# Optimization experiments

Hardware: AMD Instinct MI355X
Metric: run time of the kernel (lower is better)

## Reference

```python
import jax, jax.numpy as jnp
import numpy as np

N_NODES = 100000
N_EDGES = 1600000
IN_CH = 128
HID = 128
EPS = 1e-5


def setup_inputs() -> dict:
    key = jax.random.key(0)
    ks = jax.random.split(key, 16)
    x = jax.random.normal(ks[0], (N_NODES, IN_CH), dtype=jnp.float32)
    edge_index = jax.random.randint(ks[1], (2, N_EDGES), 0, N_NODES, dtype=jnp.int64)
    dims = [(IN_CH, HID), (HID, HID), (HID, HID // 2)]
    params = {}
    for i, (di, do) in enumerate(dims):
        params[f'w{i}'] = jax.random.normal(ks[2 + i], (di, do), dtype=jnp.float32) * (1.0 / np.sqrt(di))
        params[f'b{i}'] = jnp.zeros((do,), dtype=jnp.float32)
        params[f'g{i}'] = jnp.ones((do,), dtype=jnp.float32)
        params[f'be{i}'] = jnp.zeros((do,), dtype=jnp.float32)
    params['wc1'] = jax.random.normal(ks[8], (HID // 2, 32), dtype=jnp.float32) * (1.0 / np.sqrt(HID // 2))
    params['bc1'] = jnp.zeros((32,), dtype=jnp.float32)
    params['wc2'] = jax.random.normal(ks[9], (32, 1), dtype=jnp.float32) * (1.0 / np.sqrt(32))
    params['bc2'] = jnp.zeros((1,), dtype=jnp.float32)
    return {'x': x, 'edge_index': edge_index, **params}


def _gcn_forward(x, edge_index, w0, b0, g0, be0, w1, b1, g1, be1, w2, b2, g2, be2, wc1, bc1, wc2, bc2):
    n = x.shape[0]
    # add self-loops (GCNConv default)
    loops = jnp.arange(n, dtype=edge_index.dtype)
    src = jnp.concatenate([edge_index[0], loops])  # [E+N]
    dst = jnp.concatenate([edge_index[1], loops])
    # symmetric normalization: deg over targets (incl. self loops)
    deg = jax.ops.segment_sum(jnp.ones_like(dst, dtype=x.dtype), dst, num_segments=n)
    dis = jax.lax.rsqrt(jnp.maximum(deg, 1e-12))  # deg>=1 due to self loops
    norm = (dis[src] * dis[dst])[:, None]  # [E+N, 1]

    def layer(h, w, b, g, be):
        h = h @ w                                   # [N, d_out]
        h = jax.ops.segment_sum(h[src] * norm, dst, num_segments=n) + b
        mu = jnp.mean(h, axis=0)
        var = jnp.mean(jnp.square(h - mu), axis=0)  # biased var (torch BN)
        h = (h - mu) * jax.lax.rsqrt(var + EPS) * g + be
        return jax.nn.relu(h)                       # dropout: identity (eval)

    h = layer(x, w0, b0, g0, be0)
    h = layer(h, w1, b1, g1, be1)
    h = layer(h, w2, b2, g2, be2)
    h = jax.nn.relu(h @ wc1 + bc1)
    return (h @ wc2 + bc2)[:, 0]  # [N]


def reference(x, edge_index, w0, b0, g0, be0, w1, b1, g1, be1, w2, b2, g2, be2, wc1, bc1, wc2, bc2):
    return _gcn_forward(x, edge_index, w0, b0, g0, be0, w1, b1, g1, be1, w2, b2, g2, be2, wc1, bc1, wc2, bc2)
```

## Files before the change

### kernel.cpp

```cpp
#include <hip/hip_runtime.h>


typedef __attribute__((ext_vector_type(8))) short short8;
typedef __attribute__((ext_vector_type(4))) float f32x4;

#define BIN_SHIFT 7
#define BIN_NODES 128
#define CAPB 4096
#define CAP 64

__device__ __forceinline__ float b2f(unsigned short u) {
    return __uint_as_float(((unsigned)u) << 16);
}
__device__ __forceinline__ unsigned short f2bf(float f) {
    unsigned u = __float_as_uint(f);
    return (unsigned short)((u + 0x7fff + ((u >> 16) & 1)) >> 16);
}

__global__ __launch_bounds__(256) void part1_kernel(const int* __restrict__ eidx,
                                                    int E, int nbins, int chunk,
                                                    int* __restrict__ bin_fill,
                                                    int* __restrict__ binned) {
    __shared__ int cntS[1024];
    __shared__ int baseS[1024];
    int tid = threadIdx.x;
    for (int b = tid; b < nbins; b += 256) cntS[b] = 0;
    __syncthreads();
    int e0 = blockIdx.x * chunk;
    int e1 = min(e0 + chunk, E);
    for (int e = e0 + tid; e < e1; e += 256)
        atomicAdd(&cntS[eidx[E + e] >> BIN_SHIFT], 1);
    __syncthreads();
    for (int b = tid; b < nbins; b += 256) {
        baseS[b] = atomicAdd(&bin_fill[b], cntS[b]);
        cntS[b] = 0;
    }
    __syncthreads();
    for (int e = e0 + tid; e < e1; e += 256) {
        int d = eidx[E + e];
        int s = eidx[e];
        int b = d >> BIN_SHIFT;
        int p = baseS[b] + atomicAdd(&cntS[b], 1);
        if (p < CAPB) binned[b * CAPB + p] = (s << BIN_SHIFT) | (d & (BIN_NODES - 1));
    }
}

__global__ __launch_bounds__(256) void part2_kernel(const int* __restrict__ bin_fill,
                                                    const int* __restrict__ binned,
                                                    int N, int* __restrict__ fill,
                                                    float* __restrict__ dis,
                                                    int* __restrict__ stage) {
    __shared__ int lfill[BIN_NODES];
    int b = blockIdx.x, tid = threadIdx.x;
    if (tid < BIN_NODES) lfill[tid] = 0;
    __syncthreads();
    int cnt = min(bin_fill[b], CAPB);
    const int* seg = binned + b * CAPB;
    for (int i = tid; i < cnt; i += 256) {
        int v = seg[i];
        int dl = v & (BIN_NODES - 1);
        int p = atomicAdd(&lfill[dl], 1);
        int node = (b << BIN_SHIFT) + dl;
        if (p < CAP) stage[(node << 6) + p] = v >> BIN_SHIFT;
    }
    __syncthreads();
    if (tid < BIN_NODES) {
        int node = (b << BIN_SHIFT) + tid;
        if (node < N) {
            int c = lfill[tid];
            fill[node] = c;
            dis[node] = rsqrtf((float)c + 1.0f);
        }
    }
}

__global__ void wfrag_kernel(const float* __restrict__ w,
                             unsigned short* __restrict__ wf, int total, int C) {
    int tid = blockIdx.x * 256 + threadIdx.x;
    if (tid >= total) return;
    int j = tid & 7;
    int lane = (tid >> 3) & 63;
    int q = (tid >> 9) & 3;
    int n_tile = tid >> 11;
    int k = q * 32 + (lane >> 4) * 8 + j;
    int n = n_tile * 16 + (lane & 15);
    wf[tid] = f2bf(w[k * C + n]);
}

__device__ __forceinline__ void load8(const float* p, float4& lo, float4& hi) {
    lo = *(const float4*)p;
    hi = *(const float4*)(p + 4);
}
__device__ __forceinline__ void load8(const unsigned short* p, float4& lo, float4& hi) {
    int4 q = *(const int4*)p;
    lo = make_float4(__uint_as_float((unsigned)q.x << 16),
                     __uint_as_float((unsigned)q.x & 0xffff0000u),
                     __uint_as_float((unsigned)q.y << 16),
                     __uint_as_float((unsigned)q.y & 0xffff0000u));
    hi = make_float4(__uint_as_float((unsigned)q.z << 16),
                     __uint_as_float((unsigned)q.z & 0xffff0000u),
                     __uint_as_float((unsigned)q.w << 16),
                     __uint_as_float((unsigned)q.w & 0xffff0000u));
}

template <int C, typename InT>
__global__ __launch_bounds__(256, 5) void mfma_gemm_kernel(
    const InT* __restrict__ xin, const unsigned short* __restrict__ wf,
    const float* __restrict__ scale, const float* __restrict__ shift,
    const float* __restrict__ dis, unsigned short* __restrict__ out, int N) {
    constexpr int NT = C / 16;
    constexpr int WFRAGS = NT * 4 * 64;
    __shared__ short8 ws[WFRAGS];
    int tid = threadIdx.x;
    for (int i = tid; i < WFRAGS; i += 256) ws[i] = ((const short8*)wf)[i];

    int lane = tid & 63;
    int wave = tid >> 6;
    int m0 = blockIdx.x * 64 + wave * 16;
    int r15 = lane & 15, r4 = lane >> 4;
    f32x4 acc[NT];
#pragma unroll
    for (int t = 0; t < NT; t++) acc[t] = (f32x4){0.f, 0.f, 0.f, 0.f};
    int row0 = m0 + r15;
    int row0c = min(row0, N - 1);
    __syncthreads();

#pragma unroll
    for (int q = 0; q < 4; q++) {
        int kb = q * 32 + r4 * 8;
        float4 a0l, a0h;
        load8(xin + (size_t)row0c * 128 + kb, a0l, a0h);
        if (scale) {
            float4 scl = *(const float4*)&scale[kb];
            float4 sch = *(const float4*)&scale[kb + 4];
            float4 shl = *(const float4*)&shift[kb];
            float4 shh = *(const float4*)&shift[kb + 4];
            a0l.x = fmaxf(a0l.x * scl.x + shl.x, 0.f);
            a0l.y = fmaxf(a0l.y * scl.y + shl.y, 0.f);
            a0l.z = fmaxf(a0l.z * scl.z + shl.z, 0.f);
            a0l.w = fmaxf(a0l.w * scl.w + shl.w, 0.f);
            a0h.x = fmaxf(a0h.x * sch.x + shh.x, 0.f);
            a0h.y = fmaxf(a0h.y * sch.y + shh.y, 0.f);
            a0h.z = fmaxf(a0h.z * sch.z + shh.z, 0.f);
            a0h.w = fmaxf(a0h.w * sch.w + shh.w, 0.f);
        }
        short8 a0;
        a0[0] = (short)f2bf(a0l.x); a0[1] = (short)f2bf(a0l.y);
        a0[2] = (short)f2bf(a0l.z); a0[3] = (short)f2bf(a0l.w);
        a0[4] = (short)f2bf(a0h.x); a0[5] = (short)f2bf(a0h.y);
        a0[6] = (short)f2bf(a0h.z); a0[7] = (short)f2bf(a0h.w);
#pragma unroll
        for (int nt = 0; nt < NT; nt++) {
            short8 b = ws[(nt * 4 + q) * 64 + lane];
            acc[nt] = __builtin_amdgcn_mfma_f32_16x16x32_bf16(a0, b, acc[nt], 0, 0, 0);
        }
    }
    float d0r[4];
#pragma unroll
    for (int r = 0; r < 4; r++) {
        int rowa = m0 + r4 * 4 + r;
        d0r[r] = (rowa < N) ? dis[rowa] : 0.f;
    }
#pragma unroll
    for (int nt = 0; nt < NT; nt++) {
        int col = nt * 16 + r15;
#pragma unroll
        for (int r = 0; r < 4; r++) {
            int rowa = m0 + r4 * 4 + r;
            if (rowa < N) out[(size_t)rowa * C + col] = f2bf(acc[nt][r] * d0r[r]);
        }
    }
}

__global__ __launch_bounds__(256) void agg128_kernel(
    const unsigned short* __restrict__ h, const int* __restrict__ fill,
    const int* __restrict__ stage, const float* __restrict__ dis,
    unsigned short* __restrict__ out, int N) {
    int lane = threadIdx.x & 63;
    int node = blockIdx.x * 4 + (threadIdx.x >> 6);
    if (node >= N) return;
    float dn = dis[node];
    ushort2 sv = ((const ushort2*)(h + (size_t)node * 128))[lane];
    float2 acc = make_float2(b2f(sv.x), b2f(sv.y));
    int ne = min(fill[node], CAP);
    int pk = (lane < ne) ? stage[(node << 6) + lane] : 0;
    int j = 0;
    for (; j + 16 <= ne; j += 16) {
        ushort2 a[16];
#pragma unroll
        for (int t = 0; t < 16; t++) {
            int s = __builtin_amdgcn_readlane(pk, j + t);
            a[t] = ((const ushort2*)(h + (size_t)s * 128))[lane];
        }
#pragma unroll
        for (int t = 0; t < 16; t++) { acc.x += b2f(a[t].x); acc.y += b2f(a[t].y); }
    }
    for (; j + 8 <= ne; j += 8) {
        ushort2 a[8];
#pragma unroll
        for (int t = 0; t < 8; t++) {
            int s = __builtin_amdgcn_readlane(pk, j + t);
            a[t] = ((const ushort2*)(h + (size_t)s * 128))[lane];
        }
#pragma unroll
        for (int t = 0; t < 8; t++) { acc.x += b2f(a[t].x); acc.y += b2f(a[t].y); }
    }
    for (; j + 4 <= ne; j += 4) {
        ushort2 a[4];
#pragma unroll
        for (int t = 0; t < 4; t++) {
            int s = __builtin_amdgcn_readlane(pk, j + t);
            a[t] = ((const ushort2*)(h + (size_t)s * 128))[lane];
        }
#pragma unroll
        for (int t = 0; t < 4; t++) { acc.x += b2f(a[t].x); acc.y += b2f(a[t].y); }
    }
    for (; j < ne; j++) {
        int s = __builtin_amdgcn_readlane(pk, j);
        ushort2 a = ((const ushort2*)(h + (size_t)s * 128))[lane];
        acc.x += b2f(a.x);
        acc.y += b2f(a.y);
    }
    ((ushort2*)(out + (size_t)node * 128))[lane] =
        make_ushort2(f2bf(acc.x * dn), f2bf(acc.y * dn));
}

__global__ __launch_bounds__(256) void agg64_kernel(
    const unsigned short* __restrict__ h, const int* __restrict__ fill,
    const int* __restrict__ stage, const float* __restrict__ dis,
    unsigned short* __restrict__ out, int N) {
    int lane = threadIdx.x & 63;
    int node = blockIdx.x * 4 + (threadIdx.x >> 6);
    if (node >= N) return;
    int half = lane >> 5, ch = lane & 31;
    float dn = dis[node];
    float2 acc = make_float2(0.f, 0.f);
    if (half == 0) {
        ushort2 sv = ((const ushort2*)(h + (size_t)node * 64))[ch];
        acc.x = b2f(sv.x);
        acc.y = b2f(sv.y);
    }
    int ne = min(fill[node], CAP);
    int pk = (lane < ne) ? stage[(node << 6) + lane] : 0;
    int j = 0;
    for (; j + 16 <= ne; j += 16) {
        ushort2 a[8];
#pragma unroll
        for (int t = 0; t < 8; t++) {
            int s = __shfl(pk, j + 2 * t + half);
            a[t] = ((const ushort2*)(h + (size_t)s * 64))[ch];
        }
#pragma unroll
        for (int t = 0; t < 8; t++) { acc.x += b2f(a[t].x); acc.y += b2f(a[t].y); }
    }
    for (; j + 8 <= ne; j += 8) {
        ushort2 a[4];
#pragma unroll
        for (int t = 0; t < 4; t++) {
            int s = __shfl(pk, j + 2 * t + half);
            a[t] = ((const ushort2*)(h + (size_t)s * 64))[ch];
        }
#pragma unroll
        for (int t = 0; t < 4; t++) { acc.x += b2f(a[t].x); acc.y += b2f(a[t].y); }
    }
    for (; j < ne; j += 2) {
        int jj = j + half;
        int s = __shfl(pk, jj);
        bool v = jj < ne;
        ushort2 a = ((const ushort2*)(h + (size_t)s * 64))[ch];
        acc.x += v ? b2f(a.x) : 0.f;
        acc.y += v ? b2f(a.y) : 0.f;
    }
    acc.x += __shfl_down(acc.x, 32);
    acc.y += __shfl_down(acc.y, 32);
    if (half == 0)
        ((ushort2*)(out + (size_t)node * 64))[ch] =
            make_ushort2(f2bf(acc.x * dn), f2bf(acc.y * dn));
}

template <int C>
__global__ __launch_bounds__(256) void stats_kernel(const unsigned short* __restrict__ h,
                                                    int N, float* __restrict__ sums) {
    constexpr int R = 256 / C;
    int c = threadIdx.x % C;
    int rg = threadIdx.x / C;
    float s = 0.f, s2 = 0.f;
    for (int n = blockIdx.x * R + rg; n < N; n += gridDim.x * R) {
        float v = b2f(h[(size_t)n * C + c]);
        s += v;
        s2 += v * v;
    }
    __shared__ float red[256], red2[256];
    red[threadIdx.x] = s;
    red2[threadIdx.x] = s2;
    __syncthreads();
    if (rg == 0) {
#pragma unroll
        for (int r = 1; r < R; r++) {
            s += red[r * C + c];
            s2 += red2[r * C + c];
        }
        atomicAdd(&sums[c], s);
        atomicAdd(&sums[C + c], s2);
    }
}

template <int C>
__global__ void finalize_kernel(const float* __restrict__ sums,
                                const float* __restrict__ g,
                                const float* __restrict__ be, int N,
                                float* __restrict__ scale, float* __restrict__ shift) {
    int c = threadIdx.x;
    float inv_n = 1.0f / (float)N;
    float mean = sums[c] * inv_n;
    float var = sums[C + c] * inv_n - mean * mean;
    var = var > 0.f ? var : 0.f;
    float sc = g[c] * rsqrtf(var + 1e-5f);
    scale[c] = sc;
    shift[c] = be[c] - mean * sc;
}

__global__ __launch_bounds__(256) void head_kernel(
    const unsigned short* __restrict__ h, const float* __restrict__ scale,
    const float* __restrict__ shift, const float* __restrict__ wc1,
    const float* __restrict__ bc1, const float* __restrict__ wc2,
    const float* __restrict__ bc2, float* __restrict__ out, int N) {
    __shared__ float w1s[64 * 32];
    __shared__ float b1s[32], w2s[32], s2s[64], sh2[64];
    __shared__ float b2s;
    int tid = threadIdx.x;
    for (int i = tid; i < 64 * 32; i += 256) w1s[i] = wc1[i];
    if (tid < 32) { b1s[tid] = bc1[tid]; w2s[tid] = wc2[tid]; }
    if (tid < 64) { s2s[tid] = scale[tid]; sh2[tid] = shift[tid]; }
    if (tid == 0) b2s = bc2[0];
    __syncthreads();
    int n = blockIdx.x * 256 + tid;
    if (n >= N) return;
    float v[64];
#pragma unroll
    for (int k = 0; k < 64; k++) {
        float x = b2f(h[(size_t)n * 64 + k]) * s2s[k] + sh2[k];
        v[k] = x > 0.f ? x : 0.f;
    }
    float o = b2s;
#pragma unroll 2
    for (int j = 0; j < 32; j++) {
        float t = b1s[j];
#pragma unroll
        for (int k = 0; k < 64; k++) t += v[k] * w1s[k * 32 + j];
        t = t > 0.f ? t : 0.f;
        o += t * w2s[j];
    }
    out[n] = o;
}

extern "C" void kernel_launch(void* const* d_in, const int* in_sizes, int n_in,
                              void* d_out, int out_size, void* d_ws, size_t ws_size,
                              hipStream_t stream) {
    const float* x = (const float*)d_in[0];
    const int* eidx = (const int*)d_in[1];
    const float* w0 = (const float*)d_in[2];
    const float* g0 = (const float*)d_in[4];
    const float* be0 = (const float*)d_in[5];
    const float* w1 = (const float*)d_in[6];
    const float* g1 = (const float*)d_in[8];
    const float* be1 = (const float*)d_in[9];
    const float* w2 = (const float*)d_in[10];
    const float* g2 = (const float*)d_in[12];
    const float* be2 = (const float*)d_in[13];
    const float* wc1 = (const float*)d_in[14];
    const float* bc1 = (const float*)d_in[15];
    const float* wc2 = (const float*)d_in[16];
    const float* bc2 = (const float*)d_in[17];

    const int N = in_sizes[0] / 128;
    const int E = in_sizes[1] / 2;
    const int nbins = (N + BIN_NODES - 1) >> BIN_SHIFT;

    char* p = (char*)d_ws;
    auto alloc = [&](size_t bytes) {
        void* r = (void*)p;
        p += (bytes + 255) & ~(size_t)255;
        return r;
    };
    float* sums = (float*)alloc(3 * 256 * 4);
    int* bin_fill = (int*)alloc((size_t)nbins * 4);
    size_t zero_bytes = (size_t)(p - (char*)d_ws);
    int* fill = (int*)alloc((size_t)N * 4);
    int* binned = (int*)alloc((size_t)nbins * CAPB * 4);
    int* stage = (int*)alloc((size_t)N * CAP * 4);
    float* dis = (float*)alloc((size_t)N * 4);
    float* ss = (float*)alloc(3 * 256 * 4);
    unsigned short* hA = (unsigned short*)alloc((size_t)N * 128 * 2);
    unsigned short* hB = (unsigned short*)alloc((size_t)N * 128 * 2);
    unsigned short* wf0 = (unsigned short*)alloc(128 * 128 * 2);
    unsigned short* wf1 = (unsigned short*)alloc(128 * 128 * 2);
    unsigned short* wf2 = (unsigned short*)alloc(128 * 64 * 2);

    float* sums0 = sums, *sums1 = sums + 256, *sums2 = sums + 512;
    float* sc0 = ss, *sh0 = ss + 128;
    float* sc1 = ss + 256, *sh1 = ss + 384;
    float* sc2 = ss + 512, *sh2 = ss + 640;

    hipMemsetAsync(d_ws, 0, zero_bytes, stream);

    wfrag_kernel<<<64, 256, 0, stream>>>(w0, wf0, 128 * 128, 128);
    wfrag_kernel<<<64, 256, 0, stream>>>(w1, wf1, 128 * 128, 128);
    wfrag_kernel<<<32, 256, 0, stream>>>(w2, wf2, 128 * 64, 64);

    int p1_blocks = 256;
    int chunk = (E + p1_blocks - 1) / p1_blocks;
    part1_kernel<<<p1_blocks, 256, 0, stream>>>(eidx, E, nbins, chunk, bin_fill, binned);
    part2_kernel<<<nbins, 256, 0, stream>>>(bin_fill, binned, N, fill, dis, stage);

    int agg_grid = (N + 3) / 4;
    int gemm_grid = (N + 63) / 64;

    mfma_gemm_kernel<128, float><<<gemm_grid, 256, 0, stream>>>(x, wf0, nullptr, nullptr,
                                                                dis, hA, N);
    agg128_kernel<<<agg_grid, 256, 0, stream>>>(hA, fill, stage, dis, hB, N);
    stats_kernel<128><<<1024, 256, 0, stream>>>(hB, N, sums0);
    finalize_kernel<128><<<1, 128, 0, stream>>>(sums0, g0, be0, N, sc0, sh0);

    mfma_gemm_kernel<128, unsigned short><<<gemm_grid, 256, 0, stream>>>(
        hB, wf1, sc0, sh0, dis, hA, N);
    agg128_kernel<<<agg_grid, 256, 0, stream>>>(hA, fill, stage, dis, hB, N);
    stats_kernel<128><<<1024, 256, 0, stream>>>(hB, N, sums1);
    finalize_kernel<128><<<1, 128, 0, stream>>>(sums1, g1, be1, N, sc1, sh1);

    mfma_gemm_kernel<64, unsigned short><<<gemm_grid, 256, 0, stream>>>(
        hB, wf2, sc1, sh1, dis, hA, N);
    agg64_kernel<<<agg_grid, 256, 0, stream>>>(hA, fill, stage, dis, hB, N);
    stats_kernel<64><<<1024, 256, 0, stream>>>(hB, N, sums2);
    finalize_kernel<64><<<1, 64, 0, stream>>>(sums2, g2, be2, N, sc2, sh2);

    head_kernel<<<(N + 255) / 256, 256, 0, stream>>>(hB, sc2, sh2, wc1, bc1, wc2,
                                                     bc2, (float*)d_out, N);
}
```

Baseline: 518.1 us.

## Split 128-wide aggregation across two waves per node with one channel per lane

The 128-channel aggregation now assigns each node to two waves, each covering 64 channels with one bf16 per lane. Block indices are remapped so that both channel halves of a group of nodes run in neighbouring blocks. The 64-channel aggregation drops its two-edges-per-wave shuffle scheme and a final cross-half reduction, using one channel per lane with readlane-broadcast indices. The aim is more waves in flight and simpler gathers, at the cost of reading each neighbour index list twice and issuing narrower 2-byte loads.

```diff
diff --git a/kernel.cpp b/kernel.cpp
--- a/kernel.cpp
+++ b/kernel.cpp
@@ -177,52 +177,55 @@
     const int* __restrict__ stage, const float* __restrict__ dis,
     unsigned short* __restrict__ out, int N) {
     int lane = threadIdx.x & 63;
-    int node = blockIdx.x * 4 + (threadIdx.x >> 6);
+    int wave = threadIdx.x >> 6;
+    int r = blockIdx.x & 7;
+    int g = blockIdx.x >> 3;
+    int half = r >> 2;
+    int grp = g * 4 + (r & 3);
+    int node = grp * 4 + wave;
     if (node >= N) return;
+    int ch = half * 64 + lane;
+    const unsigned short* hc = h + ch;
     float dn = dis[node];
-    ushort2 sv = ((const ushort2*)(h + (size_t)node * 128))[lane];
-    float2 acc = make_float2(b2f(sv.x), b2f(sv.y));
+    float acc = b2f(hc[(size_t)node * 128]);
     int ne = min(fill[node], CAP);
     int pk = (lane < ne) ? stage[(node << 6) + lane] : 0;
     int j = 0;
     for (; j + 16 <= ne; j += 16) {
-        ushort2 a[16];
+        unsigned short a[16];
 #pragma unroll
         for (int t = 0; t < 16; t++) {
             int s = __builtin_amdgcn_readlane(pk, j + t);
-            a[t] = ((const ushort2*)(h + (size_t)s * 128))[lane];
-        }
-#pragma unroll
-        for (int t = 0; t < 16; t++) { acc.x += b2f(a[t].x); acc.y += b2f(a[t].y); }
+            a[t] = hc[(size_t)s * 128];
+        }
+#pragma unroll
+        for (int t = 0; t < 16; t++) acc += b2f(a[t]);
     }
     for (; j + 8 <= ne; j += 8) {
-        ushort2 a[8];
+        unsigned short a[8];
 #pragma unroll
         for (int t = 0; t < 8; t++) {
             int s = __builtin_amdgcn_readlane(pk, j + t);
-            a[t] = ((const ushort2*)(h + (size_t)s * 128))[lane];
-        }
-#pragma unroll
-        for (int t = 0; t < 8; t++) { acc.x += b2f(a[t].x); acc.y += b2f(a[t].y); }
+            a[t] = hc[(size_t)s * 128];
+        }
+#pragma unroll
+        for (int t = 0; t < 8; t++) acc += b2f(a[t]);
     }
     for (; j + 4 <= ne; j += 4) {
-        ushort2 a[4];
+        unsigned short a[4];
 #pragma unroll
         for (int t = 0; t < 4; t++) {
             int s = __builtin_amdgcn_readlane(pk, j + t);
-            a[t] = ((const ushort2*)(h + (size_t)s * 128))[lane];
-        }
-#pragma unroll
-        for (int t = 0; t < 4; t++) { acc.x += b2f(a[t].x); acc.y += b2f(a[t].y); }
+            a[t] = hc[(size_t)s * 128];
+        }
+#pragma unroll
+        for (int t = 0; t < 4; t++) acc += b2f(a[t]);
     }
     for (; j < ne; j++) {
         int s = __builtin_amdgcn_readlane(pk, j);
-        ushort2 a = ((const ushort2*)(h + (size_t)s * 128))[lane];
-        acc.x += b2f(a.x);
-        acc.y += b2f(a.y);
-    }
-    ((ushort2*)(out + (size_t)node * 128))[lane] =
-        make_ushort2(f2bf(acc.x * dn), f2bf(acc.y * dn));
+        acc += b2f(hc[(size_t)s * 128]);
+    }
+    out[(size_t)node * 128 + ch] = f2bf(acc * dn);
 }
 
 __global__ __launch_bounds__(256) void agg64_kernel(
@@ -232,50 +235,47 @@
     int lane = threadIdx.x & 63;
     int node = blockIdx.x * 4 + (threadIdx.x >> 6);
     if (node >= N) return;
-    int half = lane >> 5, ch = lane & 31;
+    const unsigned short* hc = h + lane;
     float dn = dis[node];
-    float2 acc = make_float2(0.f, 0.f);
-    if (half == 0) {
-        ushort2 sv = ((const ushort2*)(h + (size_t)node * 64))[ch];
-        acc.x = b2f(sv.x);
-        acc.y = b2f(sv.y);
-    }
+    float acc = b2f(hc[(size_t)node * 64]);
     int ne = min(fill[node], CAP);
     int pk = (lane < ne) ? stage[(node << 6) + lane] : 0;
     int j = 0;
     for (; j + 16 <= ne; j += 16) {
-        ushort2 a[8];
+        unsigned short a[16];
+#pragma unroll
+        for (int t = 0; t < 16; t++) {
+            int s = __builtin_amdgcn_readlane(pk, j + t);
+            a[t] = hc[(size_t)s * 64];
+        }
+#pragma unroll
+        for (int t = 0; t < 16; t++) acc += b2f(a[t]);
+    }
+    for (; j + 8 <= ne; j += 8) {
+        unsigned short a[8];
 #pragma unroll
         for (int t = 0; t < 8; t++) {
-            int s = __shfl(pk, j + 2 * t + half);
-            a[t] = ((const ushort2*)(h + (size_t)s * 64))[ch];
-        }
-#pragma unroll
-        for (int t = 0; t < 8; t++) { acc.x += b2f(a[t].x); acc.y += b2f(a[t].y); }
-    }
-    for (; j + 8 <= ne; j += 8) {
-        ushort2 a[4];
+            int s = __builtin_amdgcn_readlane(pk, j + t);
+            a[t] = hc[(size_t)s * 64];
+        }
+#pragma unroll
+        for (int t = 0; t < 8; t++) acc += b2f(a[t]);
+    }
+    for (; j + 4 <= ne; j += 4) {
+        unsigned short a[4];
 #pragma unroll
         for (int t = 0; t < 4; t++) {
-            int s = __shfl(pk, j + 2 * t + half);
-            a[t] = ((const ushort2*)(h + (size_t)s * 64))[ch];
-        }
-#pragma unroll
-        for (int t = 0; t < 4; t++) { acc.x += b2f(a[t].x); acc.y += b2f(a[t].y); }
-    }
-    for (; j < ne; j += 2) {
-        int jj = j + half;
-        int s = __shfl(pk, jj);
-        bool v = jj < ne;
-        ushort2 a = ((const ushort2*)(h + (size_t)s * 64))[ch];
-        acc.x += v ? b2f(a.x) : 0.f;
-        acc.y += v ? b2f(a.y) : 0.f;
-    }
-    acc.x += __shfl_down(acc.x, 32);
-    acc.y += __shfl_down(acc.y, 32);
-    if (half == 0)
-        ((ushort2*)(out + (size_t)node * 64))[ch] =
-            make_ushort2(f2bf(acc.x * dn), f2bf(acc.y * dn));
+            int s = __builtin_amdgcn_readlane(pk, j + t);
+            a[t] = hc[(size_t)s * 64];
+        }
+#pragma unroll
+        for (int t = 0; t < 4; t++) acc += b2f(a[t]);
+    }
+    for (; j < ne; j++) {
+        int s = __builtin_amdgcn_readlane(pk, j);
+        acc += b2f(hc[(size_t)s * 64]);
+    }
+    out[(size_t)node * 64 + lane] = f2bf(acc * dn);
 }
 
 template <int C>
@@ -413,24 +413,26 @@
     part1_kernel<<<p1_blocks, 256, 0, stream>>>(eidx, E, nbins, chunk, bin_fill, binned);
     part2_kernel<<<nbins, 256, 0, stream>>>(bin_fill, binned, N, fill, dis, stage);
 
-    int agg_grid = (N + 3) / 4;
+    int ngrp = (N + 3) / 4;
+    int agg128_grid = ((ngrp + 3) / 4) * 8;
+    int agg64_grid = ngrp;
     int gemm_grid = (N + 63) / 64;
 
     mfma_gemm_kernel<128, float><<<gemm_grid, 256, 0, stream>>>(x, wf0, nullptr, nullptr,
                                                                 dis, hA, N);
-    agg128_kernel<<<agg_grid, 256, 0, stream>>>(hA, fill, stage, dis, hB, N);
+    agg128_kernel<<<agg128_grid, 256, 0, stream>>>(hA, fill, stage, dis, hB, N);
     stats_kernel<128><<<1024, 256, 0, stream>>>(hB, N, sums0);
     finalize_kernel<128><<<1, 128, 0, stream>>>(sums0, g0, be0, N, sc0, sh0);
 
     mfma_gemm_kernel<128, unsigned short><<<gemm_grid, 256, 0, stream>>>(
         hB, wf1, sc0, sh0, dis, hA, N);
-    agg128_kernel<<<agg_grid, 256, 0, stream>>>(hA, fill, stage, dis, hB, N);
+    agg128_kernel<<<agg128_grid, 256, 0, stream>>>(hA, fill, stage, dis, hB, N);
     stats_kernel<128><<<1024, 256, 0, stream>>>(hB, N, sums1);
     finalize_kernel<128><<<1, 128, 0, stream>>>(sums1, g1, be1, N, sc1, sh1);
 
     mfma_gemm_kernel<64, unsigned short><<<gemm_grid, 256, 0, stream>>>(
         hB, wf2, sc1, sh1, dis, hA, N);
-    agg64_kernel<<<agg_grid, 256, 0, stream>>>(hA, fill, stage, dis, hB, N);
+    agg64_kernel<<<agg64_grid, 256, 0, stream>>>(hA, fill, stage, dis, hB, N);
     stats_kernel<64><<<1024, 256, 0, stream>>>(hB, N, sums2);
     finalize_kernel<64><<<1, 64, 0, stream>>>(sums2, g2, be2, N, sc2, sh2);
 
```

Result: slower. 548.3 us (+5.8%).
